# Optimization experiments

Measured on AMD Instinct MI355X. Metric: run time of the kernel, lower is better.

The kernel has to match this reference:

```python
import jax, jax.numpy as jnp
import numpy as np

N = 4096
K = 3          # from loss_name 'LMNN-3'
MU = 0.5       # default mu in LMNN
NUM_CLASSES = 10


def setup_inputs() -> dict:
    key = jax.random.key(0)
    k1, k2 = jax.random.split(key)
    distances_sq = jax.random.uniform(k1, (N, N), dtype=jnp.float32)
    labels = jax.random.randint(k2, (N, 1), 0, NUM_CLASSES, dtype=jnp.int32)
    return {"distances_sq": distances_sq, "labels": labels}


def lmnn(D, labels, k=K, mu=MU):
    n = D.shape[0]
    same = (labels == labels.T).astype(D.dtype)              # [n,n] same-class indicator
    cross = same * (1.0 - jnp.eye(n, dtype=D.dtype))         # exclude self-pairs
    order = jnp.argsort(D, axis=-1)                          # ascending per row
    pull_mask = jnp.take_along_axis(cross, order, axis=-1)[:, : k + 1]   # [n,k+1]
    sortD = jnp.take_along_axis(D, order, axis=-1)[:, : k + 1]           # [n,k+1]
    pull_d = sortD * pull_mask                               # masked k+1 nearest distances
    pull = jnp.sum(pull_d)
    # push: sum_{i,m,j} relu((pull_d[i,m] - D[j,i] + 1) * pull_mask[i,m] * (1 - same[j,i]))
    # vectorized form of the original per-row Python loop; hinge is [n, k+1, n]
    hinge = jax.nn.relu(
        (pull_d[:, :, None] - D.T[:, None, :] + 1.0)
        * pull_mask[:, :, None]
        * (1.0 - same.T)[:, None, :]
    )
    push = jnp.sum(hinge)
    return (1.0 - mu) * pull + mu * push


def reference(distances_sq, labels):
    # grad_reverse is identity in the forward pass
    return lmnn(distances_sq, labels)
```

## Files before the change

kernel.cpp:

```cpp
#include <hip/hip_runtime.h>

#define N 4096
#define NCLS 10
#define RPB 16
#define NCHUNK (N / RPB)
#define NSLICE 2
#define CAPS 64
#define THRESH 0.015625f
#define CRG 16
#define CRC (NCHUNK / CRG)
#define SELBLK (N / 4)
#define FOLDBLK (CRG * 4)
#define FINBLK 16

__device__ __forceinline__ bool lessvi(float v1, int i1, float v2, int i2) {
    return (v1 < v2) || (v1 == v2 && i1 < i2);
}

__device__ __forceinline__ void insert4(float vv, int ci, float tv[4], int ti[4]) {
    if (lessvi(vv, ci, tv[3], ti[3])) {
        tv[3] = vv; ti[3] = ci;
#pragma unroll
        for (int q2 = 3; q2 > 0; --q2) {
            const bool sw = lessvi(tv[q2], ti[q2], tv[q2 - 1], ti[q2 - 1]);
            const float av = tv[q2 - 1]; const int ai = ti[q2 - 1];
            tv[q2 - 1] = sw ? tv[q2] : av;
            ti[q2 - 1] = sw ? ti[q2] : ai;
            tv[q2]     = sw ? av : tv[q2];
            ti[q2]     = sw ? ai : ti[q2];
        }
    }
}

__global__ __launch_bounds__(256) void stream2d(const float* __restrict__ D,
                                                const int* __restrict__ labels,
                                                float* __restrict__ pdiff,
                                                float* __restrict__ cand_v,
                                                int* __restrict__ cand_i,
                                                int* __restrict__ cand_cnt,
                                                float* __restrict__ out) {
    __shared__ int   scnt[RPB];
    __shared__ float lv[RPB][CAPS];
    __shared__ int   li[RPB][CAPS];

    const int tid   = threadIdx.x;
    const int lane  = tid & 63;
    const int wave  = tid >> 6;
    const int slice = blockIdx.x & (NSLICE - 1);
    const int chunk = blockIdx.x >> 1;
    const int r0    = chunk * RPB;
    const int c0    = slice * 2048 + tid * 4;
    const int c1    = c0 + 1024;

    if (blockIdx.x == 0 && tid == 0) out[0] = 0.f;
    if (tid < RPB) scnt[tid] = 0;
    __syncthreads();

    const int4 clA = *(const int4*)(labels + c0);
    const int4 clB = *(const int4*)(labels + c1);
    float4 dA = {0.f, 0.f, 0.f, 0.f};
    float4 dB = {0.f, 0.f, 0.f, 0.f};

    const float4* rb = (const float4*)(D + (size_t)r0 * N + slice * 2048);
    float4 bufA[3], bufB[3];
    bufA[0] = rb[tid];        bufB[0] = rb[tid + 256];
    bufA[1] = rb[1024 + tid]; bufB[1] = rb[1024 + tid + 256];

#pragma unroll
    for (int r = 0; r < RPB; ++r) {
        if (r + 2 < RPB) {
            bufA[(r + 2) % 3] = rb[(size_t)(r + 2) * 1024 + tid];
            bufB[(r + 2) % 3] = rb[(size_t)(r + 2) * 1024 + tid + 256];
        }
        const float4 cA = bufA[r % 3];
        const float4 cB = bufB[r % 3];
        const int rowlab = labels[r0 + r];

        dA.x += (clA.x != rowlab) ? cA.x : 0.f;
        dA.y += (clA.y != rowlab) ? cA.y : 0.f;
        dA.z += (clA.z != rowlab) ? cA.z : 0.f;
        dA.w += (clA.w != rowlab) ? cA.w : 0.f;
        dB.x += (clB.x != rowlab) ? cB.x : 0.f;
        dB.y += (clB.y != rowlab) ? cB.y : 0.f;
        dB.z += (clB.z != rowlab) ? cB.z : 0.f;
        dB.w += (clB.w != rowlab) ? cB.w : 0.f;

        const float va[4] = {cA.x, cA.y, cA.z, cA.w};
        const float vb[4] = {cB.x, cB.y, cB.z, cB.w};
#pragma unroll
        for (int e = 0; e < 4; ++e) {
            if (va[e] < THRESH) {
                const int idx = atomicAdd(&scnt[r], 1);
                if (idx < CAPS) { lv[r][idx] = va[e]; li[r][idx] = c0 + e; }
            }
        }
#pragma unroll
        for (int e = 0; e < 4; ++e) {
            if (vb[e] < THRESH) {
                const int idx = atomicAdd(&scnt[r], 1);
                if (idx < CAPS) { lv[r][idx] = vb[e]; li[r][idx] = c1 + e; }
            }
        }
    }

    *(float4*)(pdiff + (size_t)chunk * N + c0) = dA;
    *(float4*)(pdiff + (size_t)chunk * N + c1) = dB;

    __syncthreads();
    for (int rr = wave; rr < RPB; rr += 4) {
        const int c   = scnt[rr];
        const int row = r0 + rr;
        if (lane == 0) cand_cnt[(size_t)row * NSLICE + slice] = c;
        if (lane < (c < CAPS ? c : CAPS)) {
            const size_t slot = (size_t)row * (NSLICE * CAPS) + slice * CAPS + lane;
            cand_v[slot] = lv[rr][lane];
            cand_i[slot] = li[rr][lane];
        }
    }
}

__global__ __launch_bounds__(256) void select_fold(const float* __restrict__ D,
                                                   const int* __restrict__ labels,
                                                   const float* __restrict__ cand_v,
                                                   const int* __restrict__ cand_i,
                                                   const int* __restrict__ cand_cnt,
                                                   const float* __restrict__ pdiff,
                                                   float* __restrict__ pd_sum,
                                                   float* __restrict__ a_cnt,
                                                   float* __restrict__ cdiff) {
    if (blockIdx.x >= SELBLK) {
        const int fb   = blockIdx.x - SELBLK;
        const int tile = fb & 3;
        const int g    = fb >> 2;
        const int col  = tile * 1024 + threadIdx.x * 4;
        float4 acc = {0.f, 0.f, 0.f, 0.f};
#pragma unroll 8
        for (int ch = 0; ch < CRC; ++ch) {
            const float4 v = *(const float4*)(pdiff + (size_t)(g * CRC + ch) * N + col);
            acc.x += v.x; acc.y += v.y; acc.z += v.z; acc.w += v.w;
        }
        *(float4*)(cdiff + (size_t)g * N + col) = acc;
        return;
    }

    const int lane = threadIdx.x & 63;
    const int wave = threadIdx.x >> 6;
    const int row  = blockIdx.x * 4 + wave;

    const int2 cnt2 = *(const int2*)(cand_cnt + (size_t)row * NSLICE);
    const int total = cnt2.x + cnt2.y;
    const bool ok = (total >= 4) && (cnt2.x <= CAPS) && (cnt2.y <= CAPS);

    float tv[4] = {INFINITY, INFINITY, INFINITY, INFINITY};
    int   ti[4] = {0x7ffffff0, 0x7ffffff1, 0x7ffffff2, 0x7ffffff3};

    if (ok) {
        const int cs2[2] = {cnt2.x, cnt2.y};
#pragma unroll
        for (int s = 0; s < 2; ++s) {
            const size_t base = (size_t)row * (NSLICE * CAPS) + s * CAPS;
            for (int k = lane; k < cs2[s]; k += 64)
                insert4(cand_v[base + k], cand_i[base + k], tv, ti);
        }
    } else {
        const float4* rp4 = (const float4*)(D + (size_t)row * N);
        for (int s = 0; s < 16; ++s) {
            const float4 q = rp4[s * 64 + lane];
            const int cc = (s * 64 + lane) * 4;
            insert4(q.x, cc, tv, ti);
            insert4(q.y, cc + 1, tv, ti);
            insert4(q.z, cc + 2, tv, ti);
            insert4(q.w, cc + 3, tv, ti);
        }
    }

#pragma unroll
    for (int off = 1; off < 64; off <<= 1) {
        float yv[4]; int yi[4];
#pragma unroll
        for (int k = 0; k < 4; ++k) {
            yv[k] = __shfl_xor(tv[k], off);
            yi[k] = __shfl_xor(ti[k], off);
        }
        float rv[4]; int ri[4];
#pragma unroll
        for (int k = 0; k < 4; ++k) {
            const bool tm = lessvi(tv[0], ti[0], yv[0], yi[0]);
            rv[k] = tm ? tv[0] : yv[0];
            ri[k] = tm ? ti[0] : yi[0];
#pragma unroll
            for (int q2 = 0; q2 < 3; ++q2) {
                tv[q2] = tm ? tv[q2 + 1] : tv[q2];
                ti[q2] = tm ? ti[q2 + 1] : ti[q2];
                yv[q2] = tm ? yv[q2]     : yv[q2 + 1];
                yi[q2] = tm ? yi[q2]     : yi[q2 + 1];
            }
        }
#pragma unroll
        for (int k = 0; k < 4; ++k) { tv[k] = rv[k]; ti[k] = ri[k]; }
    }

    if (lane == 0) {
        const int li2 = labels[row];
        float pd = 0.f, a = 0.f;
#pragma unroll
        for (int m = 0; m < 4; ++m) {
            const int j = ti[m];
            if (j != row && labels[j] == li2) { pd += tv[m]; a += 1.f; }
        }
        pd_sum[row] = pd;
        a_cnt[row]  = a;
    }
}

__global__ __launch_bounds__(256) void final_k(const float* __restrict__ cdiff,
                                               const int* __restrict__ labels,
                                               const float* __restrict__ pd_sum,
                                               const float* __restrict__ a_cnt,
                                               float* __restrict__ out) {
    __shared__ int    cnt[NCLS];
    __shared__ double red[256];
    const int tid = threadIdx.x;
    const int col = blockIdx.x * 256 + tid;

    if (tid < NCLS) cnt[tid] = 0;
    __syncthreads();
    for (int i = tid; i < N; i += 256) atomicAdd(&cnt[labels[i]], 1);
    __syncthreads();

    float cs = 0.f;
#pragma unroll
    for (int g = 0; g < CRG; ++g)
        cs += cdiff[(size_t)g * N + col];

    const int li = labels[col];
    const double pd = (double)pd_sum[col];
    const double a  = (double)a_cnt[col];
    const double cd = (double)(N - cnt[li]);
    red[tid] = pd + cd * (pd + a) - a * (double)cs;

    __syncthreads();
    for (int s = 128; s > 0; s >>= 1) {
        if (tid < s) red[tid] += red[tid + s];
        __syncthreads();
    }
    if (tid == 0) atomicAdd(out, (float)(0.5 * red[0]));
}

extern "C" void kernel_launch(void* const* d_in, const int* in_sizes, int n_in,
                              void* d_out, int out_size, void* d_ws, size_t ws_size,
                              hipStream_t stream) {
    const float* D      = (const float*)d_in[0];
    const int*   labels = (const int*)d_in[1];
    float*       out    = (float*)d_out;

    float* pdiff    = (float*)d_ws;
    float* cdiff    = pdiff + (size_t)NCHUNK * N;
    float* pd_sum   = cdiff + (size_t)CRG * N;
    float* a_cnt    = pd_sum + N;
    float* cand_v   = a_cnt + N;
    int*   cand_i   = (int*)(cand_v + (size_t)N * NSLICE * CAPS);
    int*   cand_cnt = cand_i + (size_t)N * NSLICE * CAPS;

    stream2d<<<NCHUNK * NSLICE, 256, 0, stream>>>(D, labels, pdiff, cand_v, cand_i,
                                                  cand_cnt, out);
    select_fold<<<SELBLK + FOLDBLK, 256, 0, stream>>>(D, labels, cand_v, cand_i, cand_cnt,
                                                      pdiff, pd_sum, a_cnt, cdiff);
    final_k<<<FINBLK, 256, 0, stream>>>(cdiff, labels, pd_sum, a_cnt, out);
}
```

Before: 106.2 us.

## Fuse three LMNN kernels into one cooperative kernel with grid syncs

```diff
diff --git a/kernel.cpp b/kernel.cpp
--- a/kernel.cpp
+++ b/kernel.cpp
@@ -1,4 +1,7 @@
 #include <hip/hip_runtime.h>
+#include <hip/hip_cooperative_groups.h>
+
+namespace cg = cooperative_groups;
 
 #define N 4096
 #define NCLS 10
@@ -9,6 +12,7 @@
 #define THRESH 0.015625f
 #define CRG 16
 #define CRC (NCHUNK / CRG)
+#define NBLK (NCHUNK * NSLICE)
 #define SELBLK (N / 4)
 #define FOLDBLK (CRG * 4)
 #define FINBLK 16
@@ -29,6 +33,218 @@
             tv[q2]     = sw ? av : tv[q2];
             ti[q2]     = sw ? ai : ti[q2];
         }
+    }
+}
+
+__global__ __launch_bounds__(256, 4) void lmnn_fused(const float* __restrict__ D,
+                                                     const int* __restrict__ labels,
+                                                     float* __restrict__ pdiff,
+                                                     float* __restrict__ cand_v,
+                                                     int* __restrict__ cand_i,
+                                                     int* __restrict__ cand_cnt,
+                                                     float* __restrict__ cdiff,
+                                                     float* __restrict__ pd_sum,
+                                                     float* __restrict__ a_cnt,
+                                                     float* __restrict__ out) {
+    __shared__ int    scnt[RPB];
+    __shared__ float  lv[RPB][CAPS];
+    __shared__ int    li[RPB][CAPS];
+    __shared__ int    cls[NCLS];
+    __shared__ double red[256];
+
+    const int tid  = threadIdx.x;
+    const int lane = tid & 63;
+    const int wave = tid >> 6;
+
+    {
+        const int slice = blockIdx.x & (NSLICE - 1);
+        const int chunk = blockIdx.x >> 1;
+        const int r0    = chunk * RPB;
+        const int c0    = slice * 2048 + tid * 4;
+        const int c1    = c0 + 1024;
+
+        if (blockIdx.x == 0 && tid == 0) out[0] = 0.f;
+        if (tid < RPB) scnt[tid] = 0;
+        __syncthreads();
+
+        const int4 clA = *(const int4*)(labels + c0);
+        const int4 clB = *(const int4*)(labels + c1);
+        float4 dA = {0.f, 0.f, 0.f, 0.f};
+        float4 dB = {0.f, 0.f, 0.f, 0.f};
+
+        const float4* rb = (const float4*)(D + (size_t)r0 * N + slice * 2048);
+        float4 bufA[3], bufB[3];
+        bufA[0] = rb[tid];        bufB[0] = rb[tid + 256];
+        bufA[1] = rb[1024 + tid]; bufB[1] = rb[1024 + tid + 256];
+
+#pragma unroll
+        for (int r = 0; r < RPB; ++r) {
+            if (r + 2 < RPB) {
+                bufA[(r + 2) % 3] = rb[(size_t)(r + 2) * 1024 + tid];
+                bufB[(r + 2) % 3] = rb[(size_t)(r + 2) * 1024 + tid + 256];
+            }
+            const float4 cA = bufA[r % 3];
+            const float4 cB = bufB[r % 3];
+            const int rowlab = labels[r0 + r];
+
+            dA.x += (clA.x != rowlab) ? cA.x : 0.f;
+            dA.y += (clA.y != rowlab) ? cA.y : 0.f;
+            dA.z += (clA.z != rowlab) ? cA.z : 0.f;
+            dA.w += (clA.w != rowlab) ? cA.w : 0.f;
+            dB.x += (clB.x != rowlab) ? cB.x : 0.f;
+            dB.y += (clB.y != rowlab) ? cB.y : 0.f;
+            dB.z += (clB.z != rowlab) ? cB.z : 0.f;
+            dB.w += (clB.w != rowlab) ? cB.w : 0.f;
+
+            const float va[4] = {cA.x, cA.y, cA.z, cA.w};
+            const float vb[4] = {cB.x, cB.y, cB.z, cB.w};
+#pragma unroll
+            for (int e = 0; e < 4; ++e) {
+                if (va[e] < THRESH) {
+                    const int idx = atomicAdd(&scnt[r], 1);
+                    if (idx < CAPS) { lv[r][idx] = va[e]; li[r][idx] = c0 + e; }
+                }
+            }
+#pragma unroll
+            for (int e = 0; e < 4; ++e) {
+                if (vb[e] < THRESH) {
+                    const int idx = atomicAdd(&scnt[r], 1);
+                    if (idx < CAPS) { lv[r][idx] = vb[e]; li[r][idx] = c1 + e; }
+                }
+            }
+        }
+
+        *(float4*)(pdiff + (size_t)chunk * N + c0) = dA;
+        *(float4*)(pdiff + (size_t)chunk * N + c1) = dB;
+
+        __syncthreads();
+        for (int rr = wave; rr < RPB; rr += 4) {
+            const int c   = scnt[rr];
+            const int row = r0 + rr;
+            if (lane == 0) cand_cnt[(size_t)row * NSLICE + slice] = c;
+            if (lane < (c < CAPS ? c : CAPS)) {
+                const size_t slot = (size_t)row * (NSLICE * CAPS) + slice * CAPS + lane;
+                cand_v[slot] = lv[rr][lane];
+                cand_i[slot] = li[rr][lane];
+            }
+        }
+    }
+
+    cg::this_grid().sync();
+
+    {
+#pragma unroll
+        for (int uu = 0; uu < 2; ++uu) {
+            const int row = blockIdx.x * 8 + uu * 4 + wave;
+
+            const int2 cnt2 = *(const int2*)(cand_cnt + (size_t)row * NSLICE);
+            const int total = cnt2.x + cnt2.y;
+            const bool ok = (total >= 4) && (cnt2.x <= CAPS) && (cnt2.y <= CAPS);
+
+            float tv[4] = {INFINITY, INFINITY, INFINITY, INFINITY};
+            int   ti[4] = {0x7ffffff0, 0x7ffffff1, 0x7ffffff2, 0x7ffffff3};
+
+            if (ok) {
+                const int cs2[2] = {cnt2.x, cnt2.y};
+#pragma unroll
+                for (int s = 0; s < 2; ++s) {
+                    const size_t base = (size_t)row * (NSLICE * CAPS) + s * CAPS;
+                    for (int k = lane; k < cs2[s]; k += 64)
+                        insert4(cand_v[base + k], cand_i[base + k], tv, ti);
+                }
+            } else {
+                const float4* rp4 = (const float4*)(D + (size_t)row * N);
+                for (int s = 0; s < 16; ++s) {
+                    const float4 q = rp4[s * 64 + lane];
+                    const int cc = (s * 64 + lane) * 4;
+                    insert4(q.x, cc, tv, ti);
+                    insert4(q.y, cc + 1, tv, ti);
+                    insert4(q.z, cc + 2, tv, ti);
+                    insert4(q.w, cc + 3, tv, ti);
+                }
+            }
+
+#pragma unroll
+            for (int off = 1; off < 64; off <<= 1) {
+                float yv[4]; int yi[4];
+#pragma unroll
+                for (int k = 0; k < 4; ++k) {
+                    yv[k] = __shfl_xor(tv[k], off);
+                    yi[k] = __shfl_xor(ti[k], off);
+                }
+                float rv[4]; int ri[4];
+#pragma unroll
+                for (int k = 0; k < 4; ++k) {
+                    const bool tm = lessvi(tv[0], ti[0], yv[0], yi[0]);
+                    rv[k] = tm ? tv[0] : yv[0];
+                    ri[k] = tm ? ti[0] : yi[0];
+#pragma unroll
+                    for (int q2 = 0; q2 < 3; ++q2) {
+                        tv[q2] = tm ? tv[q2 + 1] : tv[q2];
+                        ti[q2] = tm ? ti[q2 + 1] : ti[q2];
+                        yv[q2] = tm ? yv[q2]     : yv[q2 + 1];
+                        yi[q2] = tm ? yi[q2]     : yi[q2 + 1];
+                    }
+                }
+#pragma unroll
+                for (int k = 0; k < 4; ++k) { tv[k] = rv[k]; ti[k] = ri[k]; }
+            }
+
+            if (lane == 0) {
+                const int li2 = labels[row];
+                float pd = 0.f, a = 0.f;
+#pragma unroll
+                for (int m = 0; m < 4; ++m) {
+                    const int j = ti[m];
+                    if (j != row && labels[j] == li2) { pd += tv[m]; a += 1.f; }
+                }
+                pd_sum[row] = pd;
+                a_cnt[row]  = a;
+            }
+        }
+
+        if (blockIdx.x < FOLDBLK) {
+            const int fb   = blockIdx.x;
+            const int tile = fb & 3;
+            const int g    = fb >> 2;
+            const int col  = tile * 1024 + tid * 4;
+            float4 acc = {0.f, 0.f, 0.f, 0.f};
+#pragma unroll 8
+            for (int ch = 0; ch < CRC; ++ch) {
+                const float4 v = *(const float4*)(pdiff + (size_t)(g * CRC + ch) * N + col);
+                acc.x += v.x; acc.y += v.y; acc.z += v.z; acc.w += v.w;
+            }
+            *(float4*)(cdiff + (size_t)g * N + col) = acc;
+        }
+    }
+
+    cg::this_grid().sync();
+
+    if (blockIdx.x < FINBLK) {
+        const int col = blockIdx.x * 256 + tid;
+
+        if (tid < NCLS) cls[tid] = 0;
+        __syncthreads();
+        for (int i = tid; i < N; i += 256) atomicAdd(&cls[labels[i]], 1);
+        __syncthreads();
+
+        float cs = 0.f;
+#pragma unroll
+        for (int g = 0; g < CRG; ++g)
+            cs += cdiff[(size_t)g * N + col];
+
+        const int lab = labels[col];
+        const double pd = (double)pd_sum[col];
+        const double a  = (double)a_cnt[col];
+        const double cd = (double)(N - cls[lab]);
+        red[tid] = pd + cd * (pd + a) - a * (double)cs;
+
+        __syncthreads();
+        for (int s = 128; s > 0; s >>= 1) {
+            if (tid < s) red[tid] += red[tid + s];
+            __syncthreads();
+        }
+        if (tid == 0) atomicAdd(out, (float)(0.5 * red[0]));
     }
 }
 
@@ -262,9 +478,16 @@
     int*   cand_i   = (int*)(cand_v + (size_t)N * NSLICE * CAPS);
     int*   cand_cnt = cand_i + (size_t)N * NSLICE * CAPS;
 
-    stream2d<<<NCHUNK * NSLICE, 256, 0, stream>>>(D, labels, pdiff, cand_v, cand_i,
-                                                  cand_cnt, out);
-    select_fold<<<SELBLK + FOLDBLK, 256, 0, stream>>>(D, labels, cand_v, cand_i, cand_cnt,
-                                                      pdiff, pd_sum, a_cnt, cdiff);
-    final_k<<<FINBLK, 256, 0, stream>>>(cdiff, labels, pd_sum, a_cnt, out);
-}
+    void* kargs[] = {&D, &labels, &pdiff, &cand_v, &cand_i, &cand_cnt,
+                     &cdiff, &pd_sum, &a_cnt, &out};
+    hipError_t e = hipLaunchCooperativeKernel(lmnn_fused, dim3(NBLK), dim3(256),
+                                              kargs, 0u, stream);
+    if (e != hipSuccess) {
+        stream2d<<<NBLK, 256, 0, stream>>>(D, labels, pdiff, cand_v, cand_i,
+                                           cand_cnt, out);
+        select_fold<<<SELBLK + FOLDBLK, 256, 0, stream>>>(D, labels, cand_v, cand_i,
+                                                          cand_cnt, pdiff, pd_sum,
+                                                          a_cnt, cdiff);
+        final_k<<<FINBLK, 256, 0, stream>>>(cdiff, labels, pd_sum, a_cnt, out);
+    }
+}
```

After: 257.5 us. 142% more time.

## Split stream kernel into four column slices with deeper row prefetch

Applied to the files above, without the earlier changes.

```diff
diff --git a/kernel.cpp b/kernel.cpp
--- a/kernel.cpp
+++ b/kernel.cpp
@@ -4,7 +4,8 @@
 #define NCLS 10
 #define RPB 16
 #define NCHUNK (N / RPB)
-#define NSLICE 2
+#define NSLICE 4
+#define SLICEW 1024
 #define CAPS 64
 #define THRESH 0.015625f
 #define CRG 16
@@ -47,46 +48,38 @@
     const int lane  = tid & 63;
     const int wave  = tid >> 6;
     const int slice = blockIdx.x & (NSLICE - 1);
-    const int chunk = blockIdx.x >> 1;
+    const int chunk = blockIdx.x >> 2;
     const int r0    = chunk * RPB;
-    const int c0    = slice * 2048 + tid * 4;
-    const int c1    = c0 + 1024;
+    const int c0    = slice * SLICEW + tid * 4;
 
     if (blockIdx.x == 0 && tid == 0) out[0] = 0.f;
     if (tid < RPB) scnt[tid] = 0;
     __syncthreads();
 
     const int4 clA = *(const int4*)(labels + c0);
-    const int4 clB = *(const int4*)(labels + c1);
     float4 dA = {0.f, 0.f, 0.f, 0.f};
-    float4 dB = {0.f, 0.f, 0.f, 0.f};
-
-    const float4* rb = (const float4*)(D + (size_t)r0 * N + slice * 2048);
-    float4 bufA[3], bufB[3];
-    bufA[0] = rb[tid];        bufB[0] = rb[tid + 256];
-    bufA[1] = rb[1024 + tid]; bufB[1] = rb[1024 + tid + 256];
+
+    const float4* rb = (const float4*)(D + (size_t)r0 * N + slice * SLICEW);
+    float4 buf[4];
+    buf[0] = rb[tid];
+    buf[1] = rb[1024 + tid];
+    buf[2] = rb[2048 + tid];
+    buf[3] = rb[3072 + tid];
 
 #pragma unroll
     for (int r = 0; r < RPB; ++r) {
-        if (r + 2 < RPB) {
-            bufA[(r + 2) % 3] = rb[(size_t)(r + 2) * 1024 + tid];
-            bufB[(r + 2) % 3] = rb[(size_t)(r + 2) * 1024 + tid + 256];
-        }
-        const float4 cA = bufA[r % 3];
-        const float4 cB = bufB[r % 3];
+        const float4 cA = buf[r & 3];
+        if (r + 4 < RPB)
+            buf[r & 3] = rb[(size_t)(r + 4) * 1024 + tid];
+
         const int rowlab = labels[r0 + r];
 
         dA.x += (clA.x != rowlab) ? cA.x : 0.f;
         dA.y += (clA.y != rowlab) ? cA.y : 0.f;
         dA.z += (clA.z != rowlab) ? cA.z : 0.f;
         dA.w += (clA.w != rowlab) ? cA.w : 0.f;
-        dB.x += (clB.x != rowlab) ? cB.x : 0.f;
-        dB.y += (clB.y != rowlab) ? cB.y : 0.f;
-        dB.z += (clB.z != rowlab) ? cB.z : 0.f;
-        dB.w += (clB.w != rowlab) ? cB.w : 0.f;
 
         const float va[4] = {cA.x, cA.y, cA.z, cA.w};
-        const float vb[4] = {cB.x, cB.y, cB.z, cB.w};
 #pragma unroll
         for (int e = 0; e < 4; ++e) {
             if (va[e] < THRESH) {
@@ -94,17 +87,9 @@
                 if (idx < CAPS) { lv[r][idx] = va[e]; li[r][idx] = c0 + e; }
             }
         }
-#pragma unroll
-        for (int e = 0; e < 4; ++e) {
-            if (vb[e] < THRESH) {
-                const int idx = atomicAdd(&scnt[r], 1);
-                if (idx < CAPS) { lv[r][idx] = vb[e]; li[r][idx] = c1 + e; }
-            }
-        }
     }
 
     *(float4*)(pdiff + (size_t)chunk * N + c0) = dA;
-    *(float4*)(pdiff + (size_t)chunk * N + c1) = dB;
 
     __syncthreads();
     for (int rr = wave; rr < RPB; rr += 4) {
@@ -147,19 +132,20 @@
     const int wave = threadIdx.x >> 6;
     const int row  = blockIdx.x * 4 + wave;
 
-    const int2 cnt2 = *(const int2*)(cand_cnt + (size_t)row * NSLICE);
-    const int total = cnt2.x + cnt2.y;
-    const bool ok = (total >= 4) && (cnt2.x <= CAPS) && (cnt2.y <= CAPS);
+    const int4 cnt4 = *(const int4*)(cand_cnt + (size_t)row * NSLICE);
+    const int total = cnt4.x + cnt4.y + cnt4.z + cnt4.w;
+    const bool ok = (total >= 4) && (cnt4.x <= CAPS) && (cnt4.y <= CAPS) &&
+                    (cnt4.z <= CAPS) && (cnt4.w <= CAPS);
 
     float tv[4] = {INFINITY, INFINITY, INFINITY, INFINITY};
     int   ti[4] = {0x7ffffff0, 0x7ffffff1, 0x7ffffff2, 0x7ffffff3};
 
     if (ok) {
-        const int cs2[2] = {cnt2.x, cnt2.y};
-#pragma unroll
-        for (int s = 0; s < 2; ++s) {
+        const int cs4[4] = {cnt4.x, cnt4.y, cnt4.z, cnt4.w};
+#pragma unroll
+        for (int s = 0; s < NSLICE; ++s) {
             const size_t base = (size_t)row * (NSLICE * CAPS) + s * CAPS;
-            for (int k = lane; k < cs2[s]; k += 64)
+            for (int k = lane; k < cs4[s]; k += 64)
                 insert4(cand_v[base + k], cand_i[base + k], tv, ti);
         }
     } else {
```

New measurement: 105.6 us. About the same (-0.6%).
